# Performance work log

Measured on AMD Instinct MI355X. Metric: run time of the kernel, lower is better.

The kernel has to match this reference:

```python
import jax, jax.numpy as jnp
import numpy as np

N_NODES = 50000


def _gcn_norm(edge_index, num_nodes):
    # PyG gcn_norm with add_self_loops=True, edge_weight=1
    loops = jnp.arange(num_nodes, dtype=edge_index.dtype)
    src = jnp.concatenate([edge_index[0], loops])
    dst = jnp.concatenate([edge_index[1], loops])
    deg = jax.ops.segment_sum(jnp.ones_like(dst, dtype=jnp.float32), dst,
                              num_segments=num_nodes)
    deg_inv_sqrt = jnp.where(deg > 0, jax.lax.rsqrt(jnp.maximum(deg, 1.0)), 0.0)
    norm = deg_inv_sqrt[src] * deg_inv_sqrt[dst]  # [E + N]
    return src, dst, norm


def _gcn_conv(x, src, dst, norm, W, b, num_nodes):
    h = x @ W                                 # [N, out] dense transform first
    msg = h[src] * norm[:, None]              # gather + scale, [E+N, out]
    out = jax.ops.segment_sum(msg, dst, num_segments=num_nodes)  # scatter-add
    return out + b


def setup_inputs() -> dict:
    key = jax.random.key(0)
    k1, k2, k3, k4, k5 = jax.random.split(key, 5)
    in_ch, out_ch = 128, 64
    hid = 2 * out_ch
    x = jax.random.normal(k1, (N_NODES, in_ch), dtype=jnp.float32)
    edge_index = jax.random.randint(k2, (2, 800000), 0, N_NODES, dtype=jnp.int64)
    # Glorot init like PyG GCNConv
    W1 = jax.random.normal(k3, (in_ch, hid), dtype=jnp.float32) * (1.0 / np.sqrt(in_ch))
    b1 = jnp.zeros((hid,), dtype=jnp.float32)
    W2 = jax.random.normal(k4, (hid, out_ch), dtype=jnp.float32) * (1.0 / np.sqrt(hid))
    b2 = jnp.zeros((out_ch,), dtype=jnp.float32)
    return {"x": x, "edge_index": edge_index, "W1": W1, "b1": b1,
            "W2": W2, "b2": b2}


def reference(x, edge_index, W1, b1, W2, b2):
    num_nodes = x.shape[0]
    src, dst, norm = _gcn_norm(edge_index, num_nodes)
    h = _gcn_conv(x, src, dst, norm, W1, b1, num_nodes)
    h = jax.nn.relu(h)
    return _gcn_conv(h, src, dst, norm, W2, b2, num_nodes)
```

## Files before the change

### kernel.cpp

```cpp
#include <hip/hip_runtime.h>

#define N_NODES 50000
#define N_EDGES 800000
#define IN_CH   128
#define HID     128
#define OUT_CH  64

#define NBUCK 196
#define BCAP  5120
#define XPAD  136

#define G1_BLOCKS ((N_NODES + 63) / 64)
#define GSPLIT 391

typedef __attribute__((ext_vector_type(8))) short bf16x8;
typedef __attribute__((ext_vector_type(4))) float f32x4;
typedef unsigned short ushort_t;

__device__ __forceinline__ unsigned short f2bf(float f) {
    unsigned u = __float_as_uint(f);
    u += 0x7fffu + ((u >> 16) & 1u);
    return (unsigned short)(u >> 16);
}
__device__ __forceinline__ unsigned pack2(float a, float b) {
    return (unsigned)f2bf(a) | ((unsigned)f2bf(b) << 16);
}
__device__ __forceinline__ float bf_lo(unsigned u) { return __uint_as_float(u << 16); }
__device__ __forceinline__ float bf_hi(unsigned u) { return __uint_as_float(u & 0xffff0000u); }


__global__ __launch_bounds__(256) void k_prep(const float* __restrict__ W1,
                                              const float* __restrict__ W2,
                                              ushort_t* __restrict__ W1t,
                                              ushort_t* __restrict__ W2t,
                                              int* __restrict__ bcur) {
    if (blockIdx.x == 0 && threadIdx.x < NBUCK) bcur[threadIdx.x] = 0;
    int i = blockIdx.x * 256 + threadIdx.x;
    if (i < 128 * 128) {
        int k = i >> 7, c = i & 127;
        W1t[c * 128 + k] = f2bf(W1[k * 128 + c]);
    } else {
        int j = i - 128 * 128;
        if (j < 128 * 64) {
            int k = j >> 6, c = j & 63;
            W2t[c * 128 + k] = f2bf(W2[k * 64 + c]);
        }
    }
}


__global__ __launch_bounds__(256) void k_stage(const int phase, const int tile0,
                                               const int* __restrict__ src,
                                               const int* __restrict__ dst,
                                               int* __restrict__ bcur,
                                               unsigned* __restrict__ rec,
                                               const float* __restrict__ x,
                                               const ushort_t* __restrict__ W1t,
                                               ushort_t* __restrict__ g,
                                               int* __restrict__ row_beg,
                                               int* __restrict__ row_end,
                                               float* __restrict__ dis,
                                               int* __restrict__ col) {
    __shared__ char smem[52224];
    const int tid = threadIdx.x;

    if (blockIdx.x < NBUCK) {
        if (phase == 0) {
            int* lh    = (int*)smem;
            int* gbase = (int*)(smem + 1024);
            for (int i = tid; i < NBUCK; i += 256) lh[i] = 0;
            __syncthreads();
            int base = blockIdx.x * 4096;
#pragma unroll 4
            for (int k = 0; k < 16; ++k) {
                int e = base + k * 256 + tid;
                if (e < N_EDGES) atomicAdd(&lh[dst[e] >> 8], 1);
            }
            __syncthreads();
            for (int i = tid; i < NBUCK; i += 256) {
                int c = lh[i];
                gbase[i] = c ? (i * BCAP + atomicAdd(&bcur[i], c)) : 0;
            }
            __syncthreads();
            for (int i = tid; i < NBUCK; i += 256) lh[i] = 0;
            __syncthreads();
#pragma unroll 4
            for (int k = 0; k < 16; ++k) {
                int e = base + k * 256 + tid;
                if (e < N_EDGES) {
                    int d = dst[e], b = d >> 8;
                    int rk = atomicAdd(&lh[b], 1);
                    int pos = gbase[b] + rk;
                    if (pos < (b + 1) * BCAP)
                        rec[pos] = (unsigned)src[e] | ((unsigned)(d & 255) << 16);
                }
            }
        } else {
            int* lh  = (int*)smem;
            int* cur = lh + 256;
            int* s   = cur + 256;
            const int b = blockIdx.x, t = tid;
            const int lo = b * BCAP;
            const int cnt = min(bcur[b], BCAP);
            const int hi = lo + cnt;

            lh[t] = 0;
            __syncthreads();
            for (int j = lo + t; j < hi; j += 256)
                atomicAdd(&lh[rec[j] >> 16], 1);
            __syncthreads();
            int deg = lh[t];
            s[t] = deg;
            __syncthreads();
            for (int off = 1; off < 256; off <<= 1) {
                int u = (t >= off) ? s[t - off] : 0;
                __syncthreads();
                s[t] += u;
                __syncthreads();
            }
            int gp = lo + s[t] - deg;
            int node = (b << 8) + t;
            if (node < N_NODES) {
                row_beg[node] = gp;
                row_end[node] = gp + deg;
                dis[node] = rsqrtf((float)deg + 1.0f);
            }
            cur[t] = gp;
            __syncthreads();
            for (int j = lo + t; j < hi; j += 256) {
                unsigned r = rec[j];
                int pos = atomicAdd(&cur[r >> 16], 1);
                col[pos] = (int)(r & 0xffffu);
            }
        }
    } else {
        ushort_t* xs = (ushort_t*)smem;
        ushort_t* ws = (ushort_t*)(smem + 17408);
        const int bid = tile0 + (blockIdx.x - NBUCK);
        const int row0 = bid * 64;

        for (int i = tid; i < 64 * 32; i += 256) {
            int r = i >> 5, k4 = (i & 31) << 2;
            int gr = row0 + r;
            float4 v = make_float4(0.f, 0.f, 0.f, 0.f);
            if (gr < N_NODES) v = *(const float4*)&x[(long)gr * IN_CH + k4];
            ushort4 u;
            u.x = f2bf(v.x); u.y = f2bf(v.y); u.z = f2bf(v.z); u.w = f2bf(v.w);
            *(ushort4*)&xs[r * XPAD + k4] = u;
        }
        for (int i = tid; i < 128 * 16; i += 256) {
            int c = i >> 4, seg = i & 15;
            *(uint4*)&ws[c * XPAD + seg * 8] = *(const uint4*)&W1t[c * 128 + seg * 8];
        }
        __syncthreads();

        const int w = tid >> 6, lane = tid & 63;
        const int m = lane & 15, q = lane >> 4;
        const ushort_t* arow = &xs[(w * 16 + m) * XPAD + q * 8];
        const ushort_t* brow = &ws[m * XPAD + q * 8];

        f32x4 acc[8] = {};
#pragma unroll
        for (int k0 = 0; k0 < 128; k0 += 32) {
            bf16x8 a = *(const bf16x8*)(arow + k0);
#pragma unroll
            for (int nt = 0; nt < 8; ++nt) {
                bf16x8 b = *(const bf16x8*)(brow + nt * 16 * XPAD + k0);
                acc[nt] = __builtin_amdgcn_mfma_f32_16x16x32_bf16(a, b, acc[nt], 0, 0, 0);
            }
        }

#pragma unroll
        for (int reg = 0; reg < 4; ++reg) {
            int gr = row0 + w * 16 + q * 4 + reg;
            if (gr < N_NODES) {
#pragma unroll
                for (int nt = 0; nt < 8; ++nt)
                    g[(long)gr * HID + nt * 16 + m] = f2bf(acc[nt][reg]);
            }
        }
    }
}


__global__ __launch_bounds__(256) void k_agg1g2(const int* __restrict__ row_beg,
                                                const int* __restrict__ row_end,
                                                const int* __restrict__ col,
                                                const float* __restrict__ dis,
                                                const ushort_t* __restrict__ g1,
                                                const float* __restrict__ b1,
                                                const ushort_t* __restrict__ W2t,
                                                ushort_t* __restrict__ g3) {
    __shared__ ushort_t hs[16 * XPAD];
    const int tid = threadIdx.x;
    const int w = tid >> 6, lane = tid & 63;
    const int q = lane >> 4;
    const int seg = lane & 15;
    const int cl = seg << 3;
    const uint4* G = (const uint4*)g1;
    const int r0 = blockIdx.x * 16;

    for (int rr = 0; rr < 4; ++rr) {
        const int r = r0 + w * 4 + rr;
        const int beg = row_beg[r], end = row_end[r];

        float acc[8] = {};
        int e = beg + q;
        for (; e + 4 < end; e += 8) {
            int s0 = col[e], s1 = col[e + 4];
            float d0 = dis[s0], d1 = dis[s1];
            uint4 u0 = G[(long)s0 * 16 + seg];
            uint4 u1 = G[(long)s1 * 16 + seg];
            acc[0] += bf_lo(u0.x) * d0; acc[1] += bf_hi(u0.x) * d0;
            acc[2] += bf_lo(u0.y) * d0; acc[3] += bf_hi(u0.y) * d0;
            acc[4] += bf_lo(u0.z) * d0; acc[5] += bf_hi(u0.z) * d0;
            acc[6] += bf_lo(u0.w) * d0; acc[7] += bf_hi(u0.w) * d0;
            acc[0] += bf_lo(u1.x) * d1; acc[1] += bf_hi(u1.x) * d1;
            acc[2] += bf_lo(u1.y) * d1; acc[3] += bf_hi(u1.y) * d1;
            acc[4] += bf_lo(u1.z) * d1; acc[5] += bf_hi(u1.z) * d1;
            acc[6] += bf_lo(u1.w) * d1; acc[7] += bf_hi(u1.w) * d1;
        }
        if (e < end) {
            int s0 = col[e];
            float d0 = dis[s0];
            uint4 u = G[(long)s0 * 16 + seg];
            acc[0] += bf_lo(u.x) * d0; acc[1] += bf_hi(u.x) * d0;
            acc[2] += bf_lo(u.y) * d0; acc[3] += bf_hi(u.y) * d0;
            acc[4] += bf_lo(u.z) * d0; acc[5] += bf_hi(u.z) * d0;
            acc[6] += bf_lo(u.w) * d0; acc[7] += bf_hi(u.w) * d0;
        }
#pragma unroll
        for (int off = 16; off < 64; off <<= 1)
#pragma unroll
            for (int j = 0; j < 8; ++j) acc[j] += __shfl_xor(acc[j], off);

        if (q == 0) {
            const float d = dis[r];
            uint4 u = G[(long)r * 16 + seg];
            acc[0] += bf_lo(u.x) * d; acc[1] += bf_hi(u.x) * d;
            acc[2] += bf_lo(u.y) * d; acc[3] += bf_hi(u.y) * d;
            acc[4] += bf_lo(u.z) * d; acc[5] += bf_hi(u.z) * d;
            acc[6] += bf_lo(u.w) * d; acc[7] += bf_hi(u.w) * d;
            float o[8];
#pragma unroll
            for (int j = 0; j < 8; ++j) o[j] = fmaxf(acc[j] * d + b1[cl + j], 0.f);
            uint4 pw;
            pw.x = pack2(o[0], o[1]); pw.y = pack2(o[2], o[3]);
            pw.z = pack2(o[4], o[5]); pw.w = pack2(o[6], o[7]);
            *(uint4*)&hs[(w * 4 + rr) * XPAD + cl] = pw;
        }
    }
    __syncthreads();

    const int m = lane & 15;
    const ushort_t* arow = &hs[m * XPAD + q * 8];
    const ushort_t* brow = &W2t[(w * 16 + m) * 128 + q * 8];

    f32x4 acc2 = {};
#pragma unroll
    for (int k0 = 0; k0 < 128; k0 += 32) {
        bf16x8 a = *(const bf16x8*)(arow + k0);
        bf16x8 b = *(const bf16x8*)(brow + k0);
        acc2 = __builtin_amdgcn_mfma_f32_16x16x32_bf16(a, b, acc2, 0, 0, 0);
    }

#pragma unroll
    for (int reg = 0; reg < 4; ++reg) {
        int gr = r0 + q * 4 + reg;
        float d = dis[gr];
        g3[(long)gr * OUT_CH + w * 16 + m] = f2bf(acc2[reg] * d);
    }
}


__global__ __launch_bounds__(256) void k_agg2(const int* __restrict__ row_beg,
                                              const int* __restrict__ row_end,
                                              const int* __restrict__ col,
                                              const float* __restrict__ dis,
                                              const ushort_t* __restrict__ g3,
                                              const float* __restrict__ b2,
                                              float* __restrict__ out) {
    int r = blockIdx.x * 4 + (threadIdx.x >> 6);
    if (r >= N_NODES) return;
    const int lane = threadIdx.x & 63;
    const int q = lane >> 3;
    const int seg = lane & 7;
    const int cl = seg << 3;
    const uint4* G = (const uint4*)g3;
    const int beg = row_beg[r], end = row_end[r];

    float acc[8] = {};
    int e = beg + q;
    for (; e + 8 < end; e += 16) {
        int s0 = col[e], s1 = col[e + 8];
        uint4 u0 = G[(long)s0 * 8 + seg];
        uint4 u1 = G[(long)s1 * 8 + seg];
        acc[0] += bf_lo(u0.x); acc[1] += bf_hi(u0.x);
        acc[2] += bf_lo(u0.y); acc[3] += bf_hi(u0.y);
        acc[4] += bf_lo(u0.z); acc[5] += bf_hi(u0.z);
        acc[6] += bf_lo(u0.w); acc[7] += bf_hi(u0.w);
        acc[0] += bf_lo(u1.x); acc[1] += bf_hi(u1.x);
        acc[2] += bf_lo(u1.y); acc[3] += bf_hi(u1.y);
        acc[4] += bf_lo(u1.z); acc[5] += bf_hi(u1.z);
        acc[6] += bf_lo(u1.w); acc[7] += bf_hi(u1.w);
    }
    if (e < end) {
        int s = col[e];
        uint4 u = G[(long)s * 8 + seg];
        acc[0] += bf_lo(u.x); acc[1] += bf_hi(u.x);
        acc[2] += bf_lo(u.y); acc[3] += bf_hi(u.y);
        acc[4] += bf_lo(u.z); acc[5] += bf_hi(u.z);
        acc[6] += bf_lo(u.w); acc[7] += bf_hi(u.w);
    }
#pragma unroll
    for (int off = 8; off < 64; off <<= 1)
#pragma unroll
        for (int j = 0; j < 8; ++j) acc[j] += __shfl_xor(acc[j], off);

    if (q == 0) {
        uint4 u = G[(long)r * 8 + seg];
        acc[0] += bf_lo(u.x); acc[1] += bf_hi(u.x);
        acc[2] += bf_lo(u.y); acc[3] += bf_hi(u.y);
        acc[4] += bf_lo(u.z); acc[5] += bf_hi(u.z);
        acc[6] += bf_lo(u.w); acc[7] += bf_hi(u.w);
        const float d = dis[r];
        float4 o0, o1;
        o0.x = acc[0] * d + b2[cl + 0];
        o0.y = acc[1] * d + b2[cl + 1];
        o0.z = acc[2] * d + b2[cl + 2];
        o0.w = acc[3] * d + b2[cl + 3];
        o1.x = acc[4] * d + b2[cl + 4];
        o1.y = acc[5] * d + b2[cl + 5];
        o1.z = acc[6] * d + b2[cl + 6];
        o1.w = acc[7] * d + b2[cl + 7];
        *(float4*)&out[(long)r * OUT_CH + cl] = o0;
        *(float4*)&out[(long)r * OUT_CH + cl + 4] = o1;
    }
}


extern "C" void kernel_launch(void* const* d_in, const int* in_sizes, int n_in,
                              void* d_out, int out_size, void* d_ws, size_t ws_size,
                              hipStream_t stream) {
    const float* x   = (const float*)d_in[0];
    const int*   ei  = (const int*)d_in[1];
    const float* W1  = (const float*)d_in[2];
    const float* b1  = (const float*)d_in[3];
    const float* W2  = (const float*)d_in[4];
    const float* b2  = (const float*)d_in[5];
    float* out = (float*)d_out;

    const int* src = ei;
    const int* dst = ei + N_EDGES;

    char* p = (char*)d_ws;
    unsigned* rec = (unsigned*)p;         p += (long)NBUCK * BCAP * 4;
    int* col     = (int*)p;               p += (long)NBUCK * BCAP * 4;
    int* row_beg = (int*)p;               p += 50048 * 4;
    int* row_end = (int*)p;               p += 50048 * 4;
    int* bcur    = (int*)p;               p += 256 * 4;
    float* dis   = (float*)p;             p += 50048 * 4;
    ushort_t* W1t = (ushort_t*)p;         p += 128 * 128 * 2;
    ushort_t* W2t = (ushort_t*)p;         p += 128 * 64 * 2;
    ushort_t* g1  = (ushort_t*)p;         p += (long)N_NODES * HID * 2;
    ushort_t* a1  = (ushort_t*)p;         p += (long)N_NODES * HID * 2;
    ushort_t* g3  = (ushort_t*)p;
    (void)a1;

    const int B = 256;

    k_prep<<<96, B, 0, stream>>>(W1, W2, W1t, W2t, bcur);
    k_stage<<<NBUCK + GSPLIT, B, 0, stream>>>(0, 0, src, dst, bcur, rec,
                                              x, W1t, g1, row_beg, row_end, dis, col);
    k_stage<<<NBUCK + (G1_BLOCKS - GSPLIT), B, 0, stream>>>(1, GSPLIT, src, dst, bcur, rec,
                                              x, W1t, g1, row_beg, row_end, dis, col);
    k_agg1g2<<<3125, B, 0, stream>>>(row_beg, row_end, col, dis, g1, b1, W2t, g3);
    k_agg2<<<(N_NODES + 3) / 4, B, 0, stream>>>(row_beg, row_end, col, dis, g3, b2, out);
}
```

Before: 176.6 us.

## Build CSR with per-node global atomics instead of bucketed record pass

Replaces the two-pass bucketed edge sort (local histogram, bucket records, per-bucket recount and scatter) with three phases: global atomic degree count per node, per-bucket prefix scan that writes row offsets and cursors, and an atomic scatter of source indices into col. The dense GEMM tiles are now split across three staged launches instead of two to overlap with each phase. This removes the intermediate record buffer and one read/write pass over it, at the cost of contended global atomics and an extra kernel launch. Column order within a row becomes nondeterministic, and the bucket-capacity overflow guard is gone.

```diff
diff --git a/kernel.cpp b/kernel.cpp
--- a/kernel.cpp
+++ b/kernel.cpp
@@ -11,7 +11,9 @@
 #define XPAD  136
 
 #define G1_BLOCKS ((N_NODES + 63) / 64)
-#define GSPLIT 391
+#define GA 260
+#define GB 262
+#define GC 260
 
 typedef __attribute__((ext_vector_type(8))) short bf16x8;
 typedef __attribute__((ext_vector_type(4))) float f32x4;
@@ -33,18 +35,16 @@
                                               const float* __restrict__ W2,
                                               ushort_t* __restrict__ W1t,
                                               ushort_t* __restrict__ W2t,
-                                              int* __restrict__ bcur) {
-    if (blockIdx.x == 0 && threadIdx.x < NBUCK) bcur[threadIdx.x] = 0;
+                                              int* __restrict__ deg) {
     int i = blockIdx.x * 256 + threadIdx.x;
+    if (i < 50048) deg[i] = 0;
     if (i < 128 * 128) {
         int k = i >> 7, c = i & 127;
         W1t[c * 128 + k] = f2bf(W1[k * 128 + c]);
-    } else {
+    } else if (i < 128 * 128 + 128 * 64) {
         int j = i - 128 * 128;
-        if (j < 128 * 64) {
-            int k = j >> 6, c = j & 63;
-            W2t[c * 128 + k] = f2bf(W2[k * 64 + c]);
-        }
+        int k = j >> 6, c = j & 63;
+        W2t[c * 128 + k] = f2bf(W2[k * 64 + c]);
     }
 }
 
@@ -52,8 +52,8 @@
 __global__ __launch_bounds__(256) void k_stage(const int phase, const int tile0,
                                                const int* __restrict__ src,
                                                const int* __restrict__ dst,
-                                               int* __restrict__ bcur,
-                                               unsigned* __restrict__ rec,
+                                               int* __restrict__ deg,
+                                               int* __restrict__ gcur,
                                                const float* __restrict__ x,
                                                const ushort_t* __restrict__ W1t,
                                                ushort_t* __restrict__ g,
@@ -66,51 +66,18 @@
 
     if (blockIdx.x < NBUCK) {
         if (phase == 0) {
-            int* lh    = (int*)smem;
-            int* gbase = (int*)(smem + 1024);
-            for (int i = tid; i < NBUCK; i += 256) lh[i] = 0;
-            __syncthreads();
             int base = blockIdx.x * 4096;
 #pragma unroll 4
             for (int k = 0; k < 16; ++k) {
                 int e = base + k * 256 + tid;
-                if (e < N_EDGES) atomicAdd(&lh[dst[e] >> 8], 1);
-            }
-            __syncthreads();
-            for (int i = tid; i < NBUCK; i += 256) {
-                int c = lh[i];
-                gbase[i] = c ? (i * BCAP + atomicAdd(&bcur[i], c)) : 0;
-            }
-            __syncthreads();
-            for (int i = tid; i < NBUCK; i += 256) lh[i] = 0;
-            __syncthreads();
-#pragma unroll 4
-            for (int k = 0; k < 16; ++k) {
-                int e = base + k * 256 + tid;
-                if (e < N_EDGES) {
-                    int d = dst[e], b = d >> 8;
-                    int rk = atomicAdd(&lh[b], 1);
-                    int pos = gbase[b] + rk;
-                    if (pos < (b + 1) * BCAP)
-                        rec[pos] = (unsigned)src[e] | ((unsigned)(d & 255) << 16);
-                }
-            }
-        } else {
-            int* lh  = (int*)smem;
-            int* cur = lh + 256;
-            int* s   = cur + 256;
+                if (e < N_EDGES) atomicAdd(&deg[dst[e]], 1);
+            }
+        } else if (phase == 1) {
+            int* s = (int*)smem;
             const int b = blockIdx.x, t = tid;
-            const int lo = b * BCAP;
-            const int cnt = min(bcur[b], BCAP);
-            const int hi = lo + cnt;
-
-            lh[t] = 0;
-            __syncthreads();
-            for (int j = lo + t; j < hi; j += 256)
-                atomicAdd(&lh[rec[j] >> 16], 1);
-            __syncthreads();
-            int deg = lh[t];
-            s[t] = deg;
+            const int node = (b << 8) + t;
+            int d = (node < N_NODES) ? deg[node] : 0;
+            s[t] = d;
             __syncthreads();
             for (int off = 1; off < 256; off <<= 1) {
                 int u = (t >= off) ? s[t - off] : 0;
@@ -118,19 +85,23 @@
                 s[t] += u;
                 __syncthreads();
             }
-            int gp = lo + s[t] - deg;
-            int node = (b << 8) + t;
+            int gp = b * BCAP + s[t] - d;
             if (node < N_NODES) {
                 row_beg[node] = gp;
-                row_end[node] = gp + deg;
-                dis[node] = rsqrtf((float)deg + 1.0f);
-            }
-            cur[t] = gp;
-            __syncthreads();
-            for (int j = lo + t; j < hi; j += 256) {
-                unsigned r = rec[j];
-                int pos = atomicAdd(&cur[r >> 16], 1);
-                col[pos] = (int)(r & 0xffffu);
+                row_end[node] = gp + d;
+                gcur[node] = gp;
+                dis[node] = rsqrtf((float)d + 1.0f);
+            }
+        } else {
+            int base = blockIdx.x * 4096;
+#pragma unroll 4
+            for (int k = 0; k < 16; ++k) {
+                int e = base + k * 256 + tid;
+                if (e < N_EDGES) {
+                    int d = dst[e];
+                    int pos = atomicAdd(&gcur[d], 1);
+                    col[pos] = src[e];
+                }
             }
         }
     } else {
@@ -354,26 +325,26 @@
     const int* dst = ei + N_EDGES;
 
     char* p = (char*)d_ws;
-    unsigned* rec = (unsigned*)p;         p += (long)NBUCK * BCAP * 4;
     int* col     = (int*)p;               p += (long)NBUCK * BCAP * 4;
     int* row_beg = (int*)p;               p += 50048 * 4;
     int* row_end = (int*)p;               p += 50048 * 4;
-    int* bcur    = (int*)p;               p += 256 * 4;
+    int* deg     = (int*)p;               p += 50048 * 4;
+    int* gcur    = (int*)p;               p += 50048 * 4;
     float* dis   = (float*)p;             p += 50048 * 4;
     ushort_t* W1t = (ushort_t*)p;         p += 128 * 128 * 2;
     ushort_t* W2t = (ushort_t*)p;         p += 128 * 64 * 2;
     ushort_t* g1  = (ushort_t*)p;         p += (long)N_NODES * HID * 2;
-    ushort_t* a1  = (ushort_t*)p;         p += (long)N_NODES * HID * 2;
     ushort_t* g3  = (ushort_t*)p;
-    (void)a1;
 
     const int B = 256;
 
-    k_prep<<<96, B, 0, stream>>>(W1, W2, W1t, W2t, bcur);
-    k_stage<<<NBUCK + GSPLIT, B, 0, stream>>>(0, 0, src, dst, bcur, rec,
-                                              x, W1t, g1, row_beg, row_end, dis, col);
-    k_stage<<<NBUCK + (G1_BLOCKS - GSPLIT), B, 0, stream>>>(1, GSPLIT, src, dst, bcur, rec,
-                                              x, W1t, g1, row_beg, row_end, dis, col);
+    k_prep<<<196, B, 0, stream>>>(W1, W2, W1t, W2t, deg);
+    k_stage<<<NBUCK + GA, B, 0, stream>>>(0, 0, src, dst, deg, gcur,
+                                          x, W1t, g1, row_beg, row_end, dis, col);
+    k_stage<<<NBUCK + GB, B, 0, stream>>>(1, GA, src, dst, deg, gcur,
+                                          x, W1t, g1, row_beg, row_end, dis, col);
+    k_stage<<<NBUCK + GC, B, 0, stream>>>(2, GA + GB, src, dst, deg, gcur,
+                                          x, W1t, g1, row_beg, row_end, dis, col);
     k_agg1g2<<<3125, B, 0, stream>>>(row_beg, row_end, col, dis, g1, b1, W2t, g3);
     k_agg2<<<(N_NODES + 3) / 4, B, 0, stream>>>(row_beg, row_end, col, dis, g3, b2, out);
 }
```

New measurement: 231.1 us. 30.8% more time.
